# Kernel tuning notes

Hardware: AMD Instinct MI355X
Metric: run time of the kernel (lower is better)

Reference implementation:

```python
import jax, jax.numpy as jnp
import numpy as np

B, N, F, H = 32, 1024, 128, 128
NEG_BIG = -1e10


def setup_inputs() -> dict:
    key = jax.random.key(0)
    ks = jax.random.split(key, 8)
    M_features = jax.random.normal(ks[0], (B, N, F), dtype=jnp.float32)
    adj = (jax.random.uniform(ks[1], (B, N, N)) < 0.05).astype(jnp.float32)
    eye = jnp.eye(N, dtype=jnp.float32)[None]
    M_adjacency = jnp.maximum(adj, eye)
    mask = (jnp.arange(N)[None, :] < (3 * N) // 4).astype(jnp.float32)
    mask = jnp.broadcast_to(mask, (B, N)).astype(jnp.float32)
    he = lambda k, shp: jax.random.normal(k, shp, jnp.float32) * np.sqrt(2.0 / shp[0])
    W_layer = he(ks[2], (F, H))
    b_layer = jnp.zeros((H,), jnp.float32)
    W_att_self = he(ks[3], (H, 1))
    W_att_neighbor = he(ks[4], (H, 1))
    return {"M_features": M_features, "M_adjacency": M_adjacency, "mask": mask,
            "W_layer": W_layer, "b_layer": b_layer,
            "W_att_self": W_att_self, "W_att_neighbor": W_att_neighbor}


def reference(M_features, M_adjacency, mask, W_layer, b_layer, W_att_self, W_att_neighbor):
    # hidden features: [B, N, H]
    h = jnp.einsum('bnf,fh->bnh', M_features, W_layer)
    # additive attention logits: self score + neighbor score (broadcast) -> [B, N, N]
    a_self = jnp.einsum('bnh,ho->bno', h, W_att_self)          # [B, N, 1]
    a_neigh = jnp.einsum('bnh,ho->bno', h, W_att_neighbor)     # [B, N, 1]
    logits = a_self + jnp.transpose(a_neigh, (0, 2, 1))        # [B, N, N]
    logits = jax.nn.leaky_relu(logits, negative_slope=0.2)     # tf default alpha=0.2
    logits = logits + NEG_BIG * (1.0 - M_adjacency)
    attention = jax.nn.softmax(logits, axis=-1)
    # eval mode: no dropout
    h_prime = jnp.einsum('bnm,bmh->bnh', attention, h) + b_layer[None, None, :]
    h_prime = h_prime * mask[:, :, None]
    return h_prime


if __name__ == '__main__':
    out = reference(**setup_inputs())
    print(out.shape, out.dtype)
```

## Files before the change

### kernel.cpp

```cpp
#include <hip/hip_runtime.h>
#include <math.h>

#define BATCH 32
#define NN 1024
#define FF 128
#define HH 128
#define NODES 32
#define PROW 72

typedef __attribute__((ext_vector_type(8))) short short8v;
typedef __attribute__((ext_vector_type(4))) float f32x4;

__device__ __forceinline__ unsigned short f2bf(float f) {
    unsigned u = __float_as_uint(f);
    u += 0x7fffu + ((u >> 16) & 1u);
    return (unsigned short)(u >> 16);
}

__global__ __launch_bounds__(128) void gat_hidden(
    const float* __restrict__ X,
    const float* __restrict__ W,
    const float* __restrict__ Wself,
    const float* __restrict__ Wneigh,
    unsigned short* __restrict__ g,
    float* __restrict__ a_self,
    float* __restrict__ a_neigh)
{
    __shared__ float xs[NODES][FF];
    __shared__ float hs[NODES][HH + 1];
    const int tid = threadIdx.x;
    const long base_node = (long)blockIdx.x * NODES;
    const int batch = (int)(base_node >> 10);
    const int kc = (int)((base_node & 1023) >> 5);

    const float4* X4 = (const float4*)(X + base_node * FF);
    float4* xs4 = (float4*)&xs[0][0];
#pragma unroll
    for (int k = 0; k < (NODES * FF) / (4 * 128); k++)
        xs4[k * 128 + tid] = X4[k * 128 + tid];
    __syncthreads();

    float acc[NODES];
#pragma unroll
    for (int n = 0; n < NODES; n++) acc[n] = 0.f;
    const int c = tid;
    for (int fq = 0; fq < FF / 4; fq++) {
        const float w0 = W[(4 * fq + 0) * HH + c];
        const float w1 = W[(4 * fq + 1) * HH + c];
        const float w2 = W[(4 * fq + 2) * HH + c];
        const float w3 = W[(4 * fq + 3) * HH + c];
#pragma unroll
        for (int n = 0; n < NODES; n++) {
            const float4 x4 = *(const float4*)&xs[n][4 * fq];
            acc[n] += x4.x * w0 + x4.y * w1 + x4.z * w2 + x4.w * w3;
        }
    }
    {
        const int ct = c >> 4, li = c & 15;
        unsigned short* gb = g + ((((size_t)batch * 32 + kc) * 8 + ct) * 64) * 8;
        union { uint4 q; unsigned short u[8]; } pk;
#pragma unroll
        for (int kg = 0; kg < 4; kg++) {
#pragma unroll
            for (int e = 0; e < 8; e++) pk.u[e] = f2bf(acc[kg * 8 + e]);
            *(uint4*)(gb + (kg * 16 + li) * 8) = pk.q;
        }
    }
#pragma unroll
    for (int n = 0; n < NODES; n++) hs[n][c] = acc[n];
    __syncthreads();

    if (tid < 2 * NODES) {
        const int n = tid & (NODES - 1);
        const float* wvp = (tid < NODES) ? Wself : Wneigh;
        float s = 0.f;
        for (int cc = 0; cc < HH; cc++) s += hs[n][cc] * wvp[cc];
        if (tid < NODES) a_self[base_node + n] = s;
        else             a_neigh[base_node + n] = s;
    }
}

__global__ __launch_bounds__(256) void gat_attend(
    const float* __restrict__ adj,
    const float* __restrict__ mask,
    const unsigned short* __restrict__ g,
    const float* __restrict__ a_self,
    const float* __restrict__ a_neigh,
    const float* __restrict__ bvec,
    float* __restrict__ out)
{
    const int tid = threadIdx.x;
    const int lane = tid & 63;
    const int wv = tid >> 6;
    const int b = blockIdx.x;
    const int xcd = b & 7;
    const int rest = b >> 3;
    const int batch = xcd * 4 + (rest >> 5);
    const int tile = rest & 31;
    const int r0 = batch * NN + tile * 32;

    if (mask[r0] == 0.f) {
        float4* o4 = (float4*)(out + (size_t)r0 * HH);
#pragma unroll
        for (int k = 0; k < 4; k++)
            o4[k * 256 + tid] = make_float4(0.f, 0.f, 0.f, 0.f);
        return;
    }

    __shared__ unsigned short P[2][32 * PROW];
    __shared__ float rsums[32][16];
    __shared__ float rtot[32];

    const int srow = tid >> 4;
    const int scf4 = tid & 15;
    const float4* ar0 = (const float4*)(adj + (size_t)(r0 + srow) * NN);
    const float4* ar1 = (const float4*)(adj + (size_t)(r0 + srow + 16) * NN);
    const float4* anp = (const float4*)(a_neigh + batch * NN);
    const float asl0 = a_self[r0 + srow];
    const float asl1 = a_self[r0 + srow + 16];
    const unsigned short* gb = g + (size_t)batch * 131072;

    float rsr0 = 0.f, rsr1 = 0.f;
    float4 pf_an, pf_a0, pf_a1;

#define LOADS(t)                                      \
    {                                                 \
        const int o = (t) * 16 + scf4;                \
        pf_an = anp[o];                               \
        pf_a0 = ar0[o];                               \
        pf_a1 = ar1[o];                               \
    }
#define EW(a4, n4, aslv, rsv, rr, buf)                                               \
    {                                                                                \
        union { unsigned short u[4]; uint2 q; } wq;                                  \
        float x, p;                                                                  \
        x = aslv + n4.x; p = (a4.x > 0.f) ? __expf(fmaxf(x, 0.2f * x)) : 0.f;        \
        wq.u[0] = f2bf(p); rsv += __uint_as_float((unsigned)wq.u[0] << 16);          \
        x = aslv + n4.y; p = (a4.y > 0.f) ? __expf(fmaxf(x, 0.2f * x)) : 0.f;        \
        wq.u[1] = f2bf(p); rsv += __uint_as_float((unsigned)wq.u[1] << 16);          \
        x = aslv + n4.z; p = (a4.z > 0.f) ? __expf(fmaxf(x, 0.2f * x)) : 0.f;        \
        wq.u[2] = f2bf(p); rsv += __uint_as_float((unsigned)wq.u[2] << 16);          \
        x = aslv + n4.w; p = (a4.w > 0.f) ? __expf(fmaxf(x, 0.2f * x)) : 0.f;        \
        wq.u[3] = f2bf(p); rsv += __uint_as_float((unsigned)wq.u[3] << 16);          \
        *(uint2*)&P[buf][(rr) * PROW + scf4 * 4] = wq.q;                             \
    }
#define EXPWRITE(buf)                                 \
    {                                                 \
        EW(pf_a0, pf_an, asl0, rsr0, srow, buf)       \
        EW(pf_a1, pf_an, asl1, rsr1, srow + 16, buf)  \
    }

    f32x4 acc[4];
#pragma unroll
    for (int ct = 0; ct < 4; ct++)
#pragma unroll
        for (int i = 0; i < 4; i++) acc[ct][i] = 0.f;

    LOADS(0)
    EXPWRITE(0)
    __syncthreads();

    const int li = lane & 15;
    const int kg8 = (lane >> 4) * 8;
    const int rbase = (wv & 1) * 16;
    const int cg = (wv >> 1) * 4;

    for (int it = 0; it < 16; ++it) {
        const int cur = it & 1;
        if (it < 15) LOADS(it + 1)
#pragma unroll
        for (int kcl = 0; kcl < 2; kcl++) {
            const short8v af = *(const short8v*)&P[cur][(rbase + li) * PROW + kcl * 32 + kg8];
            const int kcG = it * 2 + kcl;
#pragma unroll
            for (int ctl = 0; ctl < 4; ctl++) {
                const short8v bf = *(const short8v*)(gb + ((size_t)(kcG * 8 + cg + ctl) * 64 + lane) * 8);
                acc[ctl] = __builtin_amdgcn_mfma_f32_16x16x32_bf16(af, bf, acc[ctl], 0, 0, 0);
            }
        }
        if (it < 15) EXPWRITE(cur ^ 1)
        __syncthreads();
    }

    rsums[srow][scf4] = rsr0;
    rsums[srow + 16][scf4] = rsr1;
    __syncthreads();
    if (tid < 32) {
        float s = 0.f;
#pragma unroll
        for (int q = 0; q < 16; q++) s += rsums[tid][q];
        rtot[tid] = s;
    }
    __syncthreads();

    float invv[4];
#pragma unroll
    for (int i = 0; i < 4; i++)
        invv[i] = 1.f / rtot[rbase + (lane >> 4) * 4 + i];
#pragma unroll
    for (int ctl = 0; ctl < 4; ctl++) {
        const float bv = bvec[(cg + ctl) * 16 + li];
#pragma unroll
        for (int i = 0; i < 4; i++) {
            const int r = rbase + (lane >> 4) * 4 + i;
            out[(size_t)(r0 + r) * HH + (cg + ctl) * 16 + li] =
                acc[ctl][i] * invv[i] + bv;
        }
    }
#undef EW
#undef LOADS
#undef EXPWRITE
}

extern "C" void kernel_launch(void* const* d_in, const int* in_sizes, int n_in,
                              void* d_out, int out_size, void* d_ws, size_t ws_size,
                              hipStream_t stream) {
    const float* X      = (const float*)d_in[0];
    const float* adj    = (const float*)d_in[1];
    const float* mask   = (const float*)d_in[2];
    const float* W      = (const float*)d_in[3];
    const float* bvec   = (const float*)d_in[4];
    const float* Wself  = (const float*)d_in[5];
    const float* Wneigh = (const float*)d_in[6];
    float* out = (float*)d_out;

    char* wsb = (char*)d_ws;
    unsigned short* g = (unsigned short*)wsb;
    float* a_self  = (float*)(wsb + (size_t)BATCH * NN * HH * 2);
    float* a_neigh = a_self + (size_t)BATCH * NN;

    gat_hidden<<<(BATCH * NN) / NODES, 128, 0, stream>>>(
        X, W, Wself, Wneigh, g, a_self, a_neigh);
    gat_attend<<<1024, 256, 0, stream>>>(
        adj, mask, g, a_self, a_neigh, bvec, out);
}
```

Baseline: 60.47 us.

## Make each wavefront compute its own 16-row attention tile without block barriers

The attend kernel is reorganized so each wavefront owns a 16-row tile and half the output columns. It builds its own bf16 probability tile in a private LDS region, so every __syncthreads in the K loop is removed. Row sums are reduced with lane shuffles instead of shared-memory arrays. In exchange, each pair of wavefronts now computes the exponentials for the same rows twice (once per column half), and the loop loses the previous double-buffered overlap between exp computation and MFMA.

```diff
diff --git a/kernel.cpp b/kernel.cpp
--- a/kernel.cpp
+++ b/kernel.cpp
@@ -96,58 +96,60 @@
     const int xcd = b & 7;
     const int rest = b >> 3;
     const int batch = xcd * 4 + (rest >> 5);
-    const int tile = rest & 31;
-    const int r0 = batch * NN + tile * 32;
+    const int tile = (rest & 31) * 2 + (wv >> 1);
+    const int cg = (wv & 1) * 4;
+    const int r0 = batch * NN + tile * 16;
+
+    __shared__ unsigned short P[4][2][16 * PROW];
+    unsigned short (*pew)[16 * PROW] = P[wv];
+
+    const int lrow = lane >> 2;
+    const int lcq = lane & 3;
 
     if (mask[r0] == 0.f) {
-        float4* o4 = (float4*)(out + (size_t)r0 * HH);
-#pragma unroll
-        for (int k = 0; k < 4; k++)
-            o4[k * 256 + tid] = make_float4(0.f, 0.f, 0.f, 0.f);
+        float4* o4 = (float4*)(out + (size_t)(r0 + lrow) * HH + cg * 16 + lcq * 16);
+        o4[0] = make_float4(0.f, 0.f, 0.f, 0.f);
+        o4[1] = make_float4(0.f, 0.f, 0.f, 0.f);
+        o4[2] = make_float4(0.f, 0.f, 0.f, 0.f);
+        o4[3] = make_float4(0.f, 0.f, 0.f, 0.f);
         return;
     }
 
-    __shared__ unsigned short P[2][32 * PROW];
-    __shared__ float rsums[32][16];
-    __shared__ float rtot[32];
-
-    const int srow = tid >> 4;
-    const int scf4 = tid & 15;
-    const float4* ar0 = (const float4*)(adj + (size_t)(r0 + srow) * NN);
-    const float4* ar1 = (const float4*)(adj + (size_t)(r0 + srow + 16) * NN);
-    const float4* anp = (const float4*)(a_neigh + batch * NN);
-    const float asl0 = a_self[r0 + srow];
-    const float asl1 = a_self[r0 + srow + 16];
+    const float4* arow4 = (const float4*)(adj + (size_t)(r0 + lrow) * NN);
+    const float4* an4p  = (const float4*)(a_neigh + (size_t)batch * NN);
+    const float asl = a_self[r0 + lrow];
     const unsigned short* gb = g + (size_t)batch * 131072;
 
-    float rsr0 = 0.f, rsr1 = 0.f;
-    float4 pf_an, pf_a0, pf_a1;
-
-#define LOADS(t)                                      \
-    {                                                 \
-        const int o = (t) * 16 + scf4;                \
-        pf_an = anp[o];                               \
-        pf_a0 = ar0[o];                               \
-        pf_a1 = ar1[o];                               \
-    }
-#define EW(a4, n4, aslv, rsv, rr, buf)                                               \
+    float rs = 0.f;
+    float4 pf_a0, pf_a1, pf_a2, pf_a3, pf_n0, pf_n1, pf_n2, pf_n3;
+
+#define LOADS(t)                                              \
+    {                                                         \
+        const int o = (t) * 16 + lcq * 4;                     \
+        pf_a0 = arow4[o];     pf_a1 = arow4[o + 1];           \
+        pf_a2 = arow4[o + 2]; pf_a3 = arow4[o + 3];           \
+        pf_n0 = an4p[o];      pf_n1 = an4p[o + 1];            \
+        pf_n2 = an4p[o + 2];  pf_n3 = an4p[o + 3];            \
+    }
+#define EW4(a4, n4, off)                                                             \
     {                                                                                \
-        union { unsigned short u[4]; uint2 q; } wq;                                  \
         float x, p;                                                                  \
-        x = aslv + n4.x; p = (a4.x > 0.f) ? __expf(fmaxf(x, 0.2f * x)) : 0.f;        \
-        wq.u[0] = f2bf(p); rsv += __uint_as_float((unsigned)wq.u[0] << 16);          \
-        x = aslv + n4.y; p = (a4.y > 0.f) ? __expf(fmaxf(x, 0.2f * x)) : 0.f;        \
-        wq.u[1] = f2bf(p); rsv += __uint_as_float((unsigned)wq.u[1] << 16);          \
-        x = aslv + n4.z; p = (a4.z > 0.f) ? __expf(fmaxf(x, 0.2f * x)) : 0.f;        \
-        wq.u[2] = f2bf(p); rsv += __uint_as_float((unsigned)wq.u[2] << 16);          \
-        x = aslv + n4.w; p = (a4.w > 0.f) ? __expf(fmaxf(x, 0.2f * x)) : 0.f;        \
-        wq.u[3] = f2bf(p); rsv += __uint_as_float((unsigned)wq.u[3] << 16);          \
-        *(uint2*)&P[buf][(rr) * PROW + scf4 * 4] = wq.q;                             \
-    }
-#define EXPWRITE(buf)                                 \
-    {                                                 \
-        EW(pf_a0, pf_an, asl0, rsr0, srow, buf)       \
-        EW(pf_a1, pf_an, asl1, rsr1, srow + 16, buf)  \
+        x = asl + n4.x; p = (a4.x > 0.f) ? __expf(fmaxf(x, 0.2f * x)) : 0.f;         \
+        pk.u[(off) + 0] = f2bf(p); rs += __uint_as_float((unsigned)pk.u[(off) + 0] << 16); \
+        x = asl + n4.y; p = (a4.y > 0.f) ? __expf(fmaxf(x, 0.2f * x)) : 0.f;         \
+        pk.u[(off) + 1] = f2bf(p); rs += __uint_as_float((unsigned)pk.u[(off) + 1] << 16); \
+        x = asl + n4.z; p = (a4.z > 0.f) ? __expf(fmaxf(x, 0.2f * x)) : 0.f;         \
+        pk.u[(off) + 2] = f2bf(p); rs += __uint_as_float((unsigned)pk.u[(off) + 2] << 16); \
+        x = asl + n4.w; p = (a4.w > 0.f) ? __expf(fmaxf(x, 0.2f * x)) : 0.f;         \
+        pk.u[(off) + 3] = f2bf(p); rs += __uint_as_float((unsigned)pk.u[(off) + 3] << 16); \
+    }
+#define EXPWRITE(buf)                                                 \
+    {                                                                 \
+        union { unsigned short u[16]; uint4 q[2]; } pk;               \
+        EW4(pf_a0, pf_n0, 0)  EW4(pf_a1, pf_n1, 4)                    \
+        EW4(pf_a2, pf_n2, 8)  EW4(pf_a3, pf_n3, 12)                   \
+        uint4* dst = (uint4*)&pew[buf][lrow * PROW + lcq * 16];       \
+        dst[0] = pk.q[0]; dst[1] = pk.q[1];                           \
     }
 
     f32x4 acc[4];
@@ -155,22 +157,18 @@
     for (int ct = 0; ct < 4; ct++)
 #pragma unroll
         for (int i = 0; i < 4; i++) acc[ct][i] = 0.f;
-
-    LOADS(0)
-    EXPWRITE(0)
-    __syncthreads();
 
     const int li = lane & 15;
     const int kg8 = (lane >> 4) * 8;
-    const int rbase = (wv & 1) * 16;
-    const int cg = (wv >> 1) * 4;
-
+
+    LOADS(0)
     for (int it = 0; it < 16; ++it) {
         const int cur = it & 1;
+        EXPWRITE(cur)
         if (it < 15) LOADS(it + 1)
 #pragma unroll
         for (int kcl = 0; kcl < 2; kcl++) {
-            const short8v af = *(const short8v*)&P[cur][(rbase + li) * PROW + kcl * 32 + kg8];
+            const short8v af = *(const short8v*)&pew[cur][li * PROW + kcl * 32 + kg8];
             const int kcG = it * 2 + kcl;
 #pragma unroll
             for (int ctl = 0; ctl < 4; ctl++) {
@@ -178,37 +176,27 @@
                 acc[ctl] = __builtin_amdgcn_mfma_f32_16x16x32_bf16(af, bf, acc[ctl], 0, 0, 0);
             }
         }
-        if (it < 15) EXPWRITE(cur ^ 1)
-        __syncthreads();
-    }
-
-    rsums[srow][scf4] = rsr0;
-    rsums[srow + 16][scf4] = rsr1;
-    __syncthreads();
-    if (tid < 32) {
-        float s = 0.f;
-#pragma unroll
-        for (int q = 0; q < 16; q++) s += rsums[tid][q];
-        rtot[tid] = s;
-    }
-    __syncthreads();
-
+    }
+
+    rs += __shfl_xor(rs, 1);
+    rs += __shfl_xor(rs, 2);
     float invv[4];
 #pragma unroll
     for (int i = 0; i < 4; i++)
-        invv[i] = 1.f / rtot[rbase + (lane >> 4) * 4 + i];
+        invv[i] = 1.f / __shfl(rs, ((lane >> 4) * 4 + i) * 4);
+
 #pragma unroll
     for (int ctl = 0; ctl < 4; ctl++) {
         const float bv = bvec[(cg + ctl) * 16 + li];
 #pragma unroll
         for (int i = 0; i < 4; i++) {
-            const int r = rbase + (lane >> 4) * 4 + i;
+            const int r = (lane >> 4) * 4 + i;
             out[(size_t)(r0 + r) * HH + (cg + ctl) * 16 + li] =
                 acc[ctl][i] * invv[i] + bv;
         }
     }
-#undef EW
 #undef LOADS
+#undef EW4
 #undef EXPWRITE
 }
 
```

After: 96.45 us. 1.59x slower.
